# Kernel optimization log

Measured on AMD Instinct MI355X. Metric: run time of the kernel, lower is better.

## Reference

```python
import jax, jax.numpy as jnp
import numpy as np

C = 256; NH = 8; HD = C // NH; NL = 4; NP = 4; DFF = 1024
B = 8; NQ = 900
SHAPES = ((100, 100), (50, 50), (25, 25), (13, 13))
LEN = sum(h * w for h, w in SHAPES)


def setup_inputs() -> dict:
    key = jax.random.key(0)
    ks = jax.random.split(key, 16)
    s = 0.02
    d = {}
    d['tgt'] = jax.random.normal(ks[0], (B, NQ, C), jnp.float32)
    d['query_pos'] = jax.random.normal(ks[1], (B, NQ, C), jnp.float32)
    d['reference_points'] = jax.random.uniform(ks[2], (B, NQ, NL, 2), jnp.float32)
    d['src'] = jax.random.normal(ks[3], (B, LEN, C), jnp.float32)
    d['spatial_shapes'] = np.array(SHAPES, dtype=np.int32)
    # self-attn (nn.MultiheadAttention) params, stored [in,out]
    d['sa_in_w'] = jax.random.normal(ks[4], (C, 3 * C), jnp.float32) * s
    d['sa_in_b'] = jnp.zeros((3 * C,), jnp.float32)
    d['sa_out_w'] = jax.random.normal(ks[5], (C, C), jnp.float32) * s
    d['sa_out_b'] = jnp.zeros((C,), jnp.float32)
    d['ln2_g'] = jnp.ones((C,), jnp.float32); d['ln2_b'] = jnp.zeros((C,), jnp.float32)
    # MSDeformAttn params
    d['off_w'] = jax.random.normal(ks[6], (C, NH * NL * NP * 2), jnp.float32) * s
    d['off_b'] = jax.random.normal(ks[7], (NH * NL * NP * 2,), jnp.float32) * 0.5
    d['attw_w'] = jax.random.normal(ks[8], (C, NH * NL * NP), jnp.float32) * s
    d['attw_b'] = jnp.zeros((NH * NL * NP,), jnp.float32)
    d['val_w'] = jax.random.normal(ks[9], (C, C), jnp.float32) * s
    d['val_b'] = jnp.zeros((C,), jnp.float32)
    d['proj_w'] = jax.random.normal(ks[10], (C, C), jnp.float32) * s
    d['proj_b'] = jnp.zeros((C,), jnp.float32)
    d['ln1_g'] = jnp.ones((C,), jnp.float32); d['ln1_b'] = jnp.zeros((C,), jnp.float32)
    # FFN
    d['lin1_w'] = jax.random.normal(ks[11], (C, DFF), jnp.float32) * s
    d['lin1_b'] = jnp.zeros((DFF,), jnp.float32)
    d['lin2_w'] = jax.random.normal(ks[12], (DFF, C), jnp.float32) * s
    d['lin2_b'] = jnp.zeros((C,), jnp.float32)
    d['ln3_g'] = jnp.ones((C,), jnp.float32); d['ln3_b'] = jnp.zeros((C,), jnp.float32)
    return d


def _ln(x, g, b):
    m = jnp.mean(x, -1, keepdims=True)
    v = jnp.mean((x - m) ** 2, -1, keepdims=True)
    return (x - m) * jax.lax.rsqrt(v + 1e-5) * g + b


def _bilinear(v, loc, H, W):
    # v: [B,NH,H*W,HD]; loc: [B,NQ,NH,NP,2] normalized to [0,1]
    # matches F.grid_sample(align_corners=False, padding_mode='zeros')
    b = v.shape[0]; nq = loc.shape[1]
    x = loc[..., 0] * W - 0.5
    y = loc[..., 1] * H - 0.5
    x0 = jnp.floor(x); y0 = jnp.floor(y)
    dx = x - x0; dy = y - y0
    x0i = x0.astype(jnp.int32); y0i = y0.astype(jnp.int32)

    def gat(ix, iy):
        valid = ((ix >= 0) & (ix < W) & (iy >= 0) & (iy < H)).astype(v.dtype)
        idx = jnp.clip(iy, 0, H - 1) * W + jnp.clip(ix, 0, W - 1)  # [B,NQ,NH,NP]
        idx_t = jnp.transpose(idx, (0, 2, 1, 3)).reshape(b, NH, nq * NP)
        g = jnp.take_along_axis(v, idx_t[..., None], axis=2).reshape(b, NH, nq, NP, HD)
        return g * jnp.transpose(valid, (0, 2, 1, 3))[..., None]

    wt = lambda a: jnp.transpose(a, (0, 2, 1, 3))[..., None]
    return (gat(x0i, y0i) * wt((1 - dx) * (1 - dy))
            + gat(x0i + 1, y0i) * wt(dx * (1 - dy))
            + gat(x0i, y0i + 1) * wt((1 - dx) * dy)
            + gat(x0i + 1, y0i + 1) * wt(dx * dy))


def _msda(q, ref, src, shapes, val_w, val_b, off_w, off_b, attw_w, attw_b, proj_w, proj_b):
    b, nq, _ = q.shape
    value = jnp.transpose((src @ val_w + val_b).reshape(b, -1, NH, HD), (0, 2, 1, 3))  # [B,NH,Len,HD]
    off = (q @ off_w + off_b).reshape(b, nq, NH, NL, NP, 2)
    aw = jax.nn.softmax((q @ attw_w + attw_b).reshape(b, nq, NH, NL * NP), -1)
    aw = aw.reshape(b, nq, NH, NL, NP)
    acc = jnp.zeros((b, NH, nq, HD), q.dtype)
    start = 0
    for l, (H_, W_) in enumerate(shapes):
        norm = jnp.array([W_, H_], q.dtype)
        loc = ref[:, :, None, l, None, :] + off[:, :, :, l] / norm  # [B,NQ,NH,NP,2]
        smp = _bilinear(value[:, :, start:start + H_ * W_], loc, H_, W_)  # [B,NH,NQ,NP,HD]
        acc = acc + jnp.sum(smp * jnp.transpose(aw[:, :, :, l], (0, 2, 1, 3))[..., None], axis=3)
        start += H_ * W_
    out = jnp.transpose(acc, (0, 2, 1, 3)).reshape(b, nq, C)
    return out @ proj_w + proj_b


def _self_attn(x, pos, in_w, in_b, out_w, out_b):
    b, nq, _ = x.shape
    qk = x + pos
    q = (qk @ in_w[:, :C] + in_b[:C]).reshape(b, nq, NH, HD)
    k = (qk @ in_w[:, C:2 * C] + in_b[C:2 * C]).reshape(b, nq, NH, HD)
    v = (x @ in_w[:, 2 * C:] + in_b[2 * C:]).reshape(b, nq, NH, HD)
    att = jax.nn.softmax(jnp.einsum('bqhd,bkhd->bhqk', q, k) * (1.0 / float(np.sqrt(HD))), -1)
    o = jnp.einsum('bhqk,bkhd->bqhd', att, v).reshape(b, nq, C)
    return o @ out_w + out_b


def _forward(tgt, query_pos, reference_points, src, shapes,
             sa_in_w, sa_in_b, sa_out_w, sa_out_b, ln2_g, ln2_b,
             off_w, off_b, attw_w, attw_b, val_w, val_b, proj_w, proj_b, ln1_g, ln1_b,
             lin1_w, lin1_b, lin2_w, lin2_b, ln3_g, ln3_b):
    t2 = _self_attn(tgt, query_pos, sa_in_w, sa_in_b, sa_out_w, sa_out_b)
    t = _ln(tgt + t2, ln2_g, ln2_b)
    t2 = _msda(t + query_pos, reference_points, src, shapes,
               val_w, val_b, off_w, off_b, attw_w, attw_b, proj_w, proj_b)
    t = _ln(t + t2, ln1_g, ln1_b)
    h = jax.nn.relu(t @ lin1_w + lin1_b) @ lin2_w + lin2_b
    return _ln(t + h, ln3_g, ln3_b)


def reference(tgt, query_pos, reference_points, src, spatial_shapes,
              sa_in_w, sa_in_b, sa_out_w, sa_out_b, ln2_g, ln2_b,
              off_w, off_b, attw_w, attw_b, val_w, val_b, proj_w, proj_b, ln1_g, ln1_b,
              lin1_w, lin1_b, lin2_w, lin2_b, ln3_g, ln3_b):
    shapes = [(int(h), int(w)) for h, w in np.asarray(spatial_shapes)]
    return _forward(tgt, query_pos, reference_points, src, shapes,
                    sa_in_w, sa_in_b, sa_out_w, sa_out_b, ln2_g, ln2_b,
                    off_w, off_b, attw_w, attw_b, val_w, val_b, proj_w, proj_b, ln1_g, ln1_b,
                    lin1_w, lin1_b, lin2_w, lin2_b, ln3_g, ln3_b)
```

## Files before the change

### kernel.cpp

```cpp
#include <hip/hip_runtime.h>
#include <hip/hip_bf16.h>
#include <type_traits>

#define C_DIM 256
#define NHEAD 8
#define HDIM 32
#define NLVL 4
#define NPT 4
#define DFF_DIM 1024
#define BB 8
#define NQ_DIM 900
#define LEN_DIM 13294
#define ROWS (BB * NQ_DIM)
#define VROWS (BB * LEN_DIM)
#define VT_LD 928

typedef __attribute__((ext_vector_type(8))) short short8v;
typedef __attribute__((ext_vector_type(8))) unsigned short ushort8v;
typedef __attribute__((ext_vector_type(4))) float float4v;
typedef __attribute__((ext_vector_type(4))) unsigned short ushort4v;

__device__ __forceinline__ float bf2f(unsigned short u) {
  union { unsigned int i; float f; } v; v.i = ((unsigned int)u) << 16; return v.f;
}
__device__ __forceinline__ unsigned short f2bf(float f) {
  __hip_bfloat16 h = __float2bfloat16(f);
  return *reinterpret_cast<unsigned short*>(&h);
}

#define WCONV_BLOCKS 2048
__global__ __launch_bounds__(256) void wprep_kernel(
    const float* __restrict__ w0, const float* __restrict__ w1,
    const float* __restrict__ w2, const float* __restrict__ w3,
    const float* __restrict__ w4, const float* __restrict__ w5,
    const float* __restrict__ w6, const float* __restrict__ w7,
    unsigned short* __restrict__ out,
    const float* __restrict__ tgt, const float* __restrict__ qpos,
    unsigned short* __restrict__ tgtbf, unsigned short* __restrict__ x0bf, int n4) {
  int bid = blockIdx.x;
  if (bid < WCONV_BLOCKS) {
    const int Ks[8] = {256, 256, 256, 256, 256, 256, 256, 1024};
    const int Ns[8] = {768, 256, 256, 128, 256, 256, 1024, 256};
    const int Oo[8] = {0, 196608, 262144, 327680, 360448, 425984, 491520, 753664};
    int w = bid >> 8, bx = bid & 255;
    int K = Ks[w], N = Ns[w];
    int ntx = N >> 5, nty = K >> 5;
    if (bx >= ntx * nty) return;
    int tx = bx % ntx, ty = bx / ntx;
    const float* W = w == 0 ? w0 : w == 1 ? w1 : w == 2 ? w2 : w == 3 ? w3
                   : w == 4 ? w4 : w == 5 ? w5 : w == 6 ? w6 : w7;
    __shared__ float tile[32][33];
    int c = threadIdx.x & 31, rg = threadIdx.x >> 5;
#pragma unroll
    for (int j = 0; j < 4; ++j) {
      int k = ty * 32 + rg * 4 + j;
      tile[rg * 4 + j][c] = W[(size_t)k * N + tx * 32 + c];
    }
    __syncthreads();
    unsigned short* o = out + Oo[w];
#pragma unroll
    for (int j = 0; j < 4; ++j) {
      int n = tx * 32 + rg * 4 + j;
      o[(size_t)n * K + ty * 32 + c] = f2bf(tile[c][rg * 4 + j]);
    }
  } else {
    int i = (bid - WCONV_BLOCKS) * 256 + threadIdx.x;
    if (i < n4) {
      float4 x = reinterpret_cast<const float4*>(tgt)[i];
      float4 y = reinterpret_cast<const float4*>(qpos)[i];
      ushort4v u1, u2;
      u1[0] = f2bf(x.x); u1[1] = f2bf(x.y); u1[2] = f2bf(x.z); u1[3] = f2bf(x.w);
      u2[0] = f2bf(x.x + y.x); u2[1] = f2bf(x.y + y.y);
      u2[2] = f2bf(x.z + y.z); u2[3] = f2bf(x.w + y.w);
      *reinterpret_cast<ushort4v*>(tgtbf + (size_t)i * 4) = u1;
      *reinterpret_cast<ushort4v*>(x0bf + (size_t)i * 4) = u2;
    }
  }
}

template <typename TA, typename TO, int RELU, int VT>
__device__ __forceinline__ void gemm_body(
    unsigned short* smem,
    const TA* __restrict__ A, const TA* __restrict__ A2,
    const unsigned short* __restrict__ Wt,
    const float* __restrict__ bias, const float* __restrict__ bias2,
    TO* __restrict__ Cout, TO* __restrict__ Cout2,
    int M, int N, int K, int lda, int ldc, int ldc2, int colSplit,
    int bx, int by) {
  auto Al = reinterpret_cast<unsigned short(*)[128][40]>(smem);
  auto Wl = reinterpret_cast<unsigned short(*)[128][40]>(smem + 10240);
  const int tid = threadIdx.x;
  const int lane = tid & 63, wid = tid >> 6;
  const int g = lane >> 4, ql = lane & 15;
  const int wr = wid >> 1, wc = wid & 1;
  const int row0 = by * 128, col0 = bx * 128;

  const TA* Ause = (A2 != nullptr && col0 >= colSplit) ? A2 : A;

  float4v acc[4][4];
#pragma unroll
  for (int i = 0; i < 4; ++i)
#pragma unroll
    for (int j = 0; j < 4; ++j) acc[i][j] = (float4v){0.f, 0.f, 0.f, 0.f};

  float4 areg_f[4];
  ushort8v areg_b[2];
  ushort8v wreg[2];

  auto loadA = [&](int k0) {
    if constexpr (std::is_same<TA, float>::value) {
#pragma unroll
      for (int j = 0; j < 4; ++j) {
        int c = tid + 256 * j;
        int row = c >> 3, f4 = c & 7;
        int gr = min(row0 + row, M - 1);
        areg_f[j] = *reinterpret_cast<const float4*>(Ause + (size_t)gr * lda + k0 + f4 * 4);
      }
    } else {
#pragma unroll
      for (int j = 0; j < 2; ++j) {
        int c = tid + 256 * j;
        int row = c >> 2, ch = c & 3;
        int gr = min(row0 + row, M - 1);
        areg_b[j] = *reinterpret_cast<const ushort8v*>(
            reinterpret_cast<const unsigned short*>(Ause) + (size_t)gr * lda + k0 + ch * 8);
      }
    }
  };
  auto loadW = [&](int k0) {
#pragma unroll
    for (int j = 0; j < 2; ++j) {
      int c = tid + 256 * j;
      int row = c >> 2, ch = c & 3;
      wreg[j] = *reinterpret_cast<const ushort8v*>(
          Wt + (size_t)(col0 + row) * K + k0 + ch * 8);
    }
  };
  auto storeA = [&](int buf) {
    if constexpr (std::is_same<TA, float>::value) {
#pragma unroll
      for (int j = 0; j < 4; ++j) {
        int c = tid + 256 * j;
        int row = c >> 3, f4 = c & 7;
        ushort4v u;
        u[0] = f2bf(areg_f[j].x); u[1] = f2bf(areg_f[j].y);
        u[2] = f2bf(areg_f[j].z); u[3] = f2bf(areg_f[j].w);
        *reinterpret_cast<ushort4v*>(&Al[buf][row][f4 * 4]) = u;
      }
    } else {
#pragma unroll
      for (int j = 0; j < 2; ++j) {
        int c = tid + 256 * j;
        int row = c >> 2, ch = c & 3;
        *reinterpret_cast<ushort8v*>(&Al[buf][row][ch * 8]) = areg_b[j];
      }
    }
  };
  auto storeW = [&](int buf) {
#pragma unroll
    for (int j = 0; j < 2; ++j) {
      int c = tid + 256 * j;
      int row = c >> 2, ch = c & 3;
      *reinterpret_cast<ushort8v*>(&Wl[buf][row][ch * 8]) = wreg[j];
    }
  };

  const int nt = K >> 5;
  loadA(0); loadW(0);
  storeA(0); storeW(0);

  for (int t = 0; t < nt; ++t) {
    __syncthreads();
    if (t + 1 < nt) { loadA((t + 1) << 5); loadW((t + 1) << 5); }
    const int cur = t & 1;
    short8v af[4], bfr[4];
#pragma unroll
    for (int mi = 0; mi < 4; ++mi)
      af[mi] = *reinterpret_cast<const short8v*>(&Al[cur][wr * 64 + mi * 16 + ql][8 * g]);
#pragma unroll
    for (int ni = 0; ni < 4; ++ni)
      bfr[ni] = *reinterpret_cast<const short8v*>(&Wl[cur][wc * 64 + ni * 16 + ql][8 * g]);
#pragma unroll
    for (int mi = 0; mi < 4; ++mi)
#pragma unroll
      for (int ni = 0; ni < 4; ++ni)
        acc[mi][ni] = __builtin_amdgcn_mfma_f32_16x16x32_bf16(af[mi], bfr[ni], acc[mi][ni], 0, 0, 0);
    if (t + 1 < nt) { storeA(cur ^ 1); storeW(cur ^ 1); }
  }

  const bool sel2 = (Cout2 != nullptr && col0 >= colSplit);
  const int cbase = sel2 ? (col0 - colSplit) : col0;
  if (VT && sel2) {
    unsigned short* vTp = reinterpret_cast<unsigned short*>(Cout2);
    float bv[4];
#pragma unroll
    for (int ni = 0; ni < 4; ++ni) bv[ni] = bias2[cbase + wc * 64 + ni * 16 + ql];
#pragma unroll
    for (int mi = 0; mi < 4; ++mi) {
#pragma unroll
      for (int r = 0; r < 4; ++r) {
        int row = row0 + wr * 64 + mi * 16 + 4 * g + r;
        if (row >= M) continue;
        int bb = row / 900, rr = row - bb * 900;
#pragma unroll
        for (int ni = 0; ni < 4; ++ni) {
          int c = cbase + wc * 64 + ni * 16 + ql;
          vTp[((size_t)bb * 256 + c) * VT_LD + rr] = f2bf(acc[mi][ni][r] + bv[ni]);
        }
      }
    }
    return;
  }
  const float* bsrc = sel2 ? bias2 : bias;
  TO* outp = sel2 ? Cout2 : Cout;
  const int ldco = sel2 ? ldc2 : ldc;
  float bv[4];
#pragma unroll
  for (int ni = 0; ni < 4; ++ni) bv[ni] = bsrc[cbase + wc * 64 + ni * 16 + ql];
#pragma unroll
  for (int mi = 0; mi < 4; ++mi) {
#pragma unroll
    for (int r = 0; r < 4; ++r) {
      int row = row0 + wr * 64 + mi * 16 + 4 * g + r;
      if (row >= M) continue;
#pragma unroll
      for (int ni = 0; ni < 4; ++ni) {
        int col = cbase + wc * 64 + ni * 16 + ql;
        float v = acc[mi][ni][r] + bv[ni];
        if (RELU) v = fmaxf(v, 0.f);
        if constexpr (std::is_same<TO, float>::value) {
          outp[(size_t)row * ldco + col] = v;
        } else {
          outp[(size_t)row * ldco + col] = __float2bfloat16(v);
        }
      }
    }
  }
}

template <typename TA, typename TO, int RELU>
__global__ __launch_bounds__(256) void mfma_gemm_kernel(
    const TA* __restrict__ A, const TA* __restrict__ A2,
    const unsigned short* __restrict__ Wt,
    const float* __restrict__ bias, const float* __restrict__ bias2,
    TO* __restrict__ Cout, TO* __restrict__ Cout2,
    int M, int N, int K, int lda, int ldc, int ldc2, int colSplit) {
  __shared__ unsigned short smem[20480];
  gemm_body<TA, TO, RELU, 0>(smem, A, A2, Wt, bias, bias2, Cout, Cout2,
                             M, N, K, lda, ldc, ldc2, colSplit,
                             blockIdx.x, blockIdx.y);
}

#define QKV_BLOCKS (6 * 57)
__global__ __launch_bounds__(256) void qkv_value_kernel(
    const unsigned short* __restrict__ x0bf, const unsigned short* __restrict__ tgtbf,
    const unsigned short* __restrict__ sa_inT, const float* __restrict__ sa_in_b,
    __hip_bfloat16* __restrict__ qkbuf, __hip_bfloat16* __restrict__ vT,
    const float* __restrict__ src, const unsigned short* __restrict__ valT,
    const float* __restrict__ val_b, __hip_bfloat16* __restrict__ value) {
  __shared__ unsigned short smem[20480];
  int bid = blockIdx.x;
  if (bid < QKV_BLOCKS) {
    gemm_body<unsigned short, __hip_bfloat16, 0, 1>(
        smem, x0bf, tgtbf, sa_inT, sa_in_b, sa_in_b + 512, qkbuf, vT,
        ROWS, 768, 256, 256, 512, 0, 512, bid % 6, bid / 6);
  } else {
    int t = bid - QKV_BLOCKS;
    gemm_body<float, __hip_bfloat16, 0, 0>(
        smem, src, nullptr, valT, val_b, nullptr, value, nullptr,
        VROWS, 256, 256, 256, 256, 0, 1 << 30, t & 1, t >> 1);
  }
}

__global__ __launch_bounds__(256) void ln_fused_kernel(const float* __restrict__ x,
                                                       const float* __restrict__ y,
                                                       const float* __restrict__ gg,
                                                       const float* __restrict__ bb,
                                                       float* __restrict__ out,
                                                       unsigned short* __restrict__ out2,
                                                       const float* __restrict__ qadd) {
  int row = blockIdx.x, t = threadIdx.x;
  size_t base = (size_t)row * C_DIM + t;
  float v = x[base] + y[base];
  float s = v, s2 = v * v;
#pragma unroll
  for (int o = 32; o > 0; o >>= 1) {
    s += __shfl_xor(s, o);
    s2 += __shfl_xor(s2, o);
  }
  __shared__ float w1[4], w2[4];
  int wid = t >> 6, lane = t & 63;
  if (lane == 0) { w1[wid] = s; w2[wid] = s2; }
  __syncthreads();
  float S = w1[0] + w1[1] + w1[2] + w1[3];
  float S2 = w2[0] + w2[1] + w2[2] + w2[3];
  float mean = S * (1.f / 256.f);
  float var = S2 * (1.f / 256.f) - mean * mean;
  float rstd = rsqrtf(var + 1e-5f);
  float r = (v - mean) * rstd * gg[t] + bb[t];
  out[base] = r;
  if (out2) {
    float r2 = qadd ? (r + qadd[base]) : r;
    out2[base] = f2bf(r2);
  }
}

__global__ __launch_bounds__(256) void self_attn_mfma_kernel(
    const unsigned short* __restrict__ qk, const unsigned short* __restrict__ vT,
    unsigned short* __restrict__ out) {
  __shared__ unsigned short P_lds[4][16][32];
  const int tid = threadIdx.x;
  const int lane = tid & 63, wid = tid >> 6;
  const int g = lane >> 4, ql = lane & 15;
  const int bh = blockIdx.y;
  const int b = bh >> 3, h = bh & 7;
  const int q0 = blockIdx.x * 64 + wid * 16;
  const float scale = 0.17677669529663687f;

  const unsigned short* qk_b = qk + (size_t)b * NQ_DIM * 512;
  const int qrow = min(q0 + ql, NQ_DIM - 1);
  short8v qf = *reinterpret_cast<const short8v*>(
      qk_b + (size_t)qrow * 512 + h * HDIM + 8 * g);
  const unsigned short* kb = qk_b + 256 + h * HDIM + 8 * g;
  const unsigned short* vtb0 = vT + ((size_t)b * 256 + h * HDIM + ql) * VT_LD;
  const unsigned short* vtb1 = vtb0 + 16 * VT_LD;

  float4v o0 = {0.f, 0.f, 0.f, 0.f}, o1 = {0.f, 0.f, 0.f, 0.f};
  float m = -1e30f, lsum = 0.f;

  const int NT = 29;
  for (int kt = 0; kt < NT; ++kt) {
    const int k_base = kt * 32;
    int kr0 = min(k_base + ql, NQ_DIM - 1);
    int kr1 = min(k_base + 16 + ql, NQ_DIM - 1);
    short8v kf0 = *reinterpret_cast<const short8v*>(kb + (size_t)kr0 * 512);
    short8v kf1 = *reinterpret_cast<const short8v*>(kb + (size_t)kr1 * 512);
    float4v z = {0.f, 0.f, 0.f, 0.f};
    float4v s0 = __builtin_amdgcn_mfma_f32_16x16x32_bf16(kf0, qf, z, 0, 0, 0);
    float4v s1 = __builtin_amdgcn_mfma_f32_16x16x32_bf16(kf1, qf, z, 0, 0, 0);

    float s[8];
#pragma unroll
    for (int r = 0; r < 4; ++r) { s[r] = s0[r] * scale; s[4 + r] = s1[r] * scale; }
    if (kt == NT - 1) {
#pragma unroll
      for (int i = 0; i < 8; ++i) {
        int kk = k_base + 16 * (i >> 2) + 4 * g + (i & 3);
        if (kk >= NQ_DIM) s[i] = -1e30f;
      }
    }
    float tm = s[0];
#pragma unroll
    for (int i = 1; i < 8; ++i) tm = fmaxf(tm, s[i]);
    tm = fmaxf(tm, __shfl_xor(tm, 16));
    tm = fmaxf(tm, __shfl_xor(tm, 32));
    float mnew = fmaxf(m, tm);
    float alpha = __expf(m - mnew);
    float p[8];
    float ts = 0.f;
#pragma unroll
    for (int i = 0; i < 8; ++i) { p[i] = __expf(s[i] - mnew); ts += p[i]; }
    ts += __shfl_xor(ts, 16);
    ts += __shfl_xor(ts, 32);
    lsum = lsum * alpha + ts;
    m = mnew;

    ushort4v pp0, pp1;
#pragma unroll
    for (int r = 0; r < 4; ++r) { pp0[r] = f2bf(p[r]); pp1[r] = f2bf(p[4 + r]); }
    *reinterpret_cast<ushort4v*>(&P_lds[wid][ql][4 * g]) = pp0;
    *reinterpret_cast<ushort4v*>(&P_lds[wid][ql][16 + 4 * g]) = pp1;
    asm volatile("s_waitcnt lgkmcnt(0)" ::: "memory");
    __builtin_amdgcn_sched_barrier(0);

    o0 *= alpha;
    o1 *= alpha;

    short8v pf = *reinterpret_cast<const short8v*>(&P_lds[wid][ql][8 * g]);
    short8v vf0 = *reinterpret_cast<const short8v*>(vtb0 + k_base + 8 * g);
    short8v vf1 = *reinterpret_cast<const short8v*>(vtb1 + k_base + 8 * g);
    o0 = __builtin_amdgcn_mfma_f32_16x16x32_bf16(vf0, pf, o0, 0, 0, 0);
    o1 = __builtin_amdgcn_mfma_f32_16x16x32_bf16(vf1, pf, o1, 0, 0, 0);
  }

  float inv = 1.f / lsum;
  if (q0 + ql < NQ_DIM) {
    unsigned short* op = out + ((size_t)(b * NQ_DIM) + q0 + ql) * C_DIM + h * HDIM;
    ushort4v u0, u1;
#pragma unroll
    for (int r = 0; r < 4; ++r) { u0[r] = f2bf(o0[r] * inv); u1[r] = f2bf(o1[r] * inv); }
    *reinterpret_cast<ushort4v*>(op + 4 * g) = u0;
    *reinterpret_cast<ushort4v*>(op + 16 + 4 * g) = u1;
  }
}

__global__ __launch_bounds__(256) void softmax16_kernel(float* __restrict__ aw, int total) {
  int t = blockIdx.x * 256 + threadIdx.x;
  if (t >= total) return;
  float* p = aw + (size_t)t * 16;
  float vals[16];
  float m = -1e30f;
#pragma unroll
  for (int i = 0; i < 16; ++i) { vals[i] = p[i]; m = fmaxf(m, vals[i]); }
  float s = 0.f;
#pragma unroll
  for (int i = 0; i < 16; ++i) { vals[i] = __expf(vals[i] - m); s += vals[i]; }
  float inv = 1.f / s;
#pragma unroll
  for (int i = 0; i < 16; ++i) p[i] = vals[i] * inv;
}

__global__ __launch_bounds__(256) void msda_sample_kernel(
    const unsigned short* __restrict__ value,
    const float* __restrict__ off,
    const float* __restrict__ aw,
    const float* __restrict__ refp,
    const int* __restrict__ shapes,
    unsigned short* __restrict__ out) {
  int g = blockIdx.x * 32 + (threadIdx.x >> 3);
  int d4 = threadIdx.x & 7;
  int h = g & 7;
  int row = g >> 3;
  int b = row / NQ_DIM;
  float acc0 = 0.f, acc1 = 0.f, acc2 = 0.f, acc3 = 0.f;
  int start = 0;
  const float* offr = off + (size_t)row * 256 + h * 32;
  const float* awr  = aw + (size_t)row * 128 + h * 16;
  const float* rpr  = refp + (size_t)row * NLVL * 2;
#pragma unroll
  for (int l = 0; l < NLVL; ++l) {
    int Hl = shapes[2 * l], Wl = shapes[2 * l + 1];
    float fx = rpr[2 * l + 0] * (float)Wl - 0.5f;
    float fy = rpr[2 * l + 1] * (float)Hl - 0.5f;
    const unsigned short* vbase =
        value + ((size_t)(b * LEN_DIM + start)) * C_DIM + h * HDIM + d4 * 4;
#pragma unroll
    for (int p = 0; p < NPT; ++p) {
      float x = fx + offr[l * 8 + p * 2];
      float y = fy + offr[l * 8 + p * 2 + 1];
      float a = awr[l * 4 + p];
      float x0f = floorf(x), y0f = floorf(y);
      float dx = x - x0f, dy = y - y0f;
      int x0 = (int)x0f, y0 = (int)y0f;
      int x1 = x0 + 1, y1 = y0 + 1;
      float wx1 = dx, wx0 = 1.f - dx;
      float wy1 = dy * a, wy0 = (1.f - dy) * a;
      bool vx0 = ((unsigned)x0 < (unsigned)Wl);
      bool vx1 = ((unsigned)x1 < (unsigned)Wl);
      bool vy0 = ((unsigned)y0 < (unsigned)Hl);
      bool vy1 = ((unsigned)y1 < (unsigned)Hl);
      float w00 = (vx0 && vy0) ? wx0 * wy0 : 0.f;
      float w10 = (vx1 && vy0) ? wx1 * wy0 : 0.f;
      float w01 = (vx0 && vy1) ? wx0 * wy1 : 0.f;
      float w11 = (vx1 && vy1) ? wx1 * wy1 : 0.f;
      int x0c = min(max(x0, 0), Wl - 1), x1c = min(max(x1, 0), Wl - 1);
      int y0c = min(max(y0, 0), Hl - 1), y1c = min(max(y1, 0), Hl - 1);
      int r0 = y0c * Wl, r1 = y1c * Wl;
      ushort4v g00 = *reinterpret_cast<const ushort4v*>(vbase + ((r0 + x0c) << 8));
      ushort4v g10 = *reinterpret_cast<const ushort4v*>(vbase + ((r0 + x1c) << 8));
      ushort4v g01 = *reinterpret_cast<const ushort4v*>(vbase + ((r1 + x0c) << 8));
      ushort4v g11 = *reinterpret_cast<const ushort4v*>(vbase + ((r1 + x1c) << 8));
      acc0 += w00 * bf2f(g00[0]) + w10 * bf2f(g10[0]) + w01 * bf2f(g01[0]) + w11 * bf2f(g11[0]);
      acc1 += w00 * bf2f(g00[1]) + w10 * bf2f(g10[1]) + w01 * bf2f(g01[1]) + w11 * bf2f(g11[1]);
      acc2 += w00 * bf2f(g00[2]) + w10 * bf2f(g10[2]) + w01 * bf2f(g01[2]) + w11 * bf2f(g11[2]);
      acc3 += w00 * bf2f(g00[3]) + w10 * bf2f(g10[3]) + w01 * bf2f(g01[3]) + w11 * bf2f(g11[3]);
    }
    start += Hl * Wl;
  }
  ushort4v o;
  o[0] = f2bf(acc0); o[1] = f2bf(acc1); o[2] = f2bf(acc2); o[3] = f2bf(acc3);
  *reinterpret_cast<ushort4v*>(out + (size_t)row * C_DIM + h * HDIM + d4 * 4) = o;
}

extern "C" void kernel_launch(void* const* d_in, const int* in_sizes, int n_in,
                              void* d_out, int out_size, void* d_ws, size_t ws_size,
                              hipStream_t stream) {
  const float* tgt      = (const float*)d_in[0];
  const float* qpos     = (const float*)d_in[1];
  const float* refp     = (const float*)d_in[2];
  const float* src      = (const float*)d_in[3];
  const int*   shapes   = (const int*)d_in[4];
  const float* sa_in_w  = (const float*)d_in[5];
  const float* sa_in_b  = (const float*)d_in[6];
  const float* sa_out_w = (const float*)d_in[7];
  const float* sa_out_b = (const float*)d_in[8];
  const float* ln2_g    = (const float*)d_in[9];
  const float* ln2_b    = (const float*)d_in[10];
  const float* off_w    = (const float*)d_in[11];
  const float* off_b    = (const float*)d_in[12];
  const float* attw_w   = (const float*)d_in[13];
  const float* attw_b   = (const float*)d_in[14];
  const float* val_w    = (const float*)d_in[15];
  const float* val_b    = (const float*)d_in[16];
  const float* proj_w   = (const float*)d_in[17];
  const float* proj_b   = (const float*)d_in[18];
  const float* ln1_g    = (const float*)d_in[19];
  const float* ln1_b    = (const float*)d_in[20];
  const float* lin1_w   = (const float*)d_in[21];
  const float* lin1_b   = (const float*)d_in[22];
  const float* lin2_w   = (const float*)d_in[23];
  const float* lin2_b   = (const float*)d_in[24];
  const float* ln3_g    = (const float*)d_in[25];
  const float* ln3_b    = (const float*)d_in[26];

  char* ws = (char*)d_ws;
  size_t off_b_ws = 0;
  auto alloc = [&](size_t bytes) {
    char* p = ws + off_b_ws;
    off_b_ws += (bytes + 255) & ~(size_t)255;
    return p;
  };
  unsigned short* wT     = (unsigned short*)alloc((size_t)1015808 * 2);
  unsigned short* value  = (unsigned short*)alloc((size_t)VROWS * C_DIM * 2);
  unsigned short* qkbuf  = (unsigned short*)alloc((size_t)ROWS * 512 * 2);
  unsigned short* vTbuf  = (unsigned short*)alloc((size_t)BB * 256 * VT_LD * 2);
  unsigned short* tgtbf  = (unsigned short*)alloc((size_t)ROWS * C_DIM * 2);
  unsigned short* X0bf   = (unsigned short*)alloc((size_t)ROWS * C_DIM * 2);
  unsigned short* attnbf = (unsigned short*)alloc((size_t)ROWS * C_DIM * 2);
  unsigned short* X3bf   = (unsigned short*)alloc((size_t)ROWS * C_DIM * 2);
  unsigned short* sampbf = (unsigned short*)alloc((size_t)ROWS * C_DIM * 2);
  unsigned short* X6bf   = (unsigned short*)alloc((size_t)ROWS * C_DIM * 2);
  unsigned short* hidbf  = (unsigned short*)alloc((size_t)ROWS * DFF_DIM * 2);
  float* X1 = (float*)alloc((size_t)ROWS * C_DIM * 4);
  float* X2 = (float*)alloc((size_t)ROWS * C_DIM * 4);
  float* X4 = (float*)alloc((size_t)ROWS * C_DIM * 4);
  float* X5 = (float*)alloc((size_t)ROWS * 128 * 4);
  float* X6 = (float*)alloc((size_t)ROWS * C_DIM * 4);
  if (off_b_ws > ws_size) return;

  unsigned short* sa_inT = wT + 0;
  unsigned short* sa_outT = wT + 196608;
  unsigned short* offT   = wT + 262144;
  unsigned short* valT   = wT + 360448;
  unsigned short* projT  = wT + 425984;
  unsigned short* lin1T  = wT + 491520;
  unsigned short* lin2T  = wT + 753664;

  dim3 blk(256);
  const int MB7200 = (ROWS + 127) / 128;
  const int MBV = (VROWS + 127) / 128;
  int n4 = ROWS * C_DIM / 4;
  int prepBlocks = (n4 + 255) / 256;

  wprep_kernel<<<WCONV_BLOCKS + prepBlocks, blk, 0, stream>>>(
      sa_in_w, sa_out_w, off_w, attw_w, val_w, proj_w, lin1_w, lin2_w, wT,
      tgt, qpos, tgtbf, X0bf, n4);

  qkv_value_kernel<<<QKV_BLOCKS + 2 * MBV, blk, 0, stream>>>(
      X0bf, tgtbf, sa_inT, sa_in_b, (__hip_bfloat16*)qkbuf, (__hip_bfloat16*)vTbuf,
      src, valT, val_b, (__hip_bfloat16*)value);

  self_attn_mfma_kernel<<<dim3(15, 64), blk, 0, stream>>>(qkbuf, vTbuf, attnbf);
  mfma_gemm_kernel<unsigned short, float, 0><<<dim3(2, MB7200), blk, 0, stream>>>(
      attnbf, nullptr, sa_outT, sa_out_b, nullptr,
      X1, nullptr, ROWS, 256, 256, 256, 256, 0, 1 << 30);
  ln_fused_kernel<<<ROWS, blk, 0, stream>>>(tgt, X1, ln2_g, ln2_b, X2, X3bf, qpos);

  mfma_gemm_kernel<unsigned short, float, 0><<<dim3(3, MB7200), blk, 0, stream>>>(
      X3bf, nullptr, offT, off_b, attw_b,
      X4, X5, ROWS, 384, 256, 256, 256, 128, 256);
  softmax16_kernel<<<(ROWS * NHEAD + 255) / 256, blk, 0, stream>>>(X5, ROWS * NHEAD);
  msda_sample_kernel<<<ROWS * NHEAD / 32, blk, 0, stream>>>(
      value, X4, X5, refp, shapes, sampbf);
  mfma_gemm_kernel<unsigned short, float, 0><<<dim3(2, MB7200), blk, 0, stream>>>(
      sampbf, nullptr, projT, proj_b, nullptr,
      X1, nullptr, ROWS, 256, 256, 256, 256, 0, 1 << 30);
  ln_fused_kernel<<<ROWS, blk, 0, stream>>>(X2, X1, ln1_g, ln1_b, X6, X6bf, nullptr);

  mfma_gemm_kernel<unsigned short, __hip_bfloat16, 1><<<dim3(8, MB7200), blk, 0, stream>>>(
      X6bf, nullptr, lin1T, lin1_b, nullptr,
      (__hip_bfloat16*)hidbf, nullptr, ROWS, 1024, 256, 256, 1024, 0, 1 << 30);
  mfma_gemm_kernel<unsigned short, float, 0><<<dim3(2, MB7200), blk, 0, stream>>>(
      hidbf, nullptr, lin2T, lin2_b, nullptr,
      X1, nullptr, ROWS, 256, 1024, 1024, 256, 0, 1 << 30);
  ln_fused_kernel<<<ROWS, blk, 0, stream>>>(X6, X1, ln3_g, ln3_b, (float*)d_out, nullptr, nullptr);
}
```

Baseline: 231.9 us.

## Split V transpose into tiled kernel and widen MSDA gathers to 8 channels

The QKV GEMM epilogue used to scatter V straight into a transposed layout with strided 2-byte stores. It now writes V row-major and a separate LDS-tiled transpose kernel builds vT with coalesced accesses. Separately, the deformable-attention sampler now has each thread gather 8 bf16 channels per corner instead of 4, which halves the thread count and launches half as many blocks. The costs are an extra kernel launch, an extra buffer round trip for V, and more registers per sampling thread.

Result: faster. 225.6 us (-2.7%).

```diff
diff --git a/kernel.cpp b/kernel.cpp
--- a/kernel.cpp
+++ b/kernel.cpp
@@ -78,7 +78,7 @@
   }
 }
 
-template <typename TA, typename TO, int RELU, int VT>
+template <typename TA, typename TO, int RELU>
 __device__ __forceinline__ void gemm_body(
     unsigned short* smem,
     const TA* __restrict__ A, const TA* __restrict__ A2,
@@ -189,31 +189,10 @@
   }
 
   const bool sel2 = (Cout2 != nullptr && col0 >= colSplit);
-  const int cbase = sel2 ? (col0 - colSplit) : col0;
-  if (VT && sel2) {
-    unsigned short* vTp = reinterpret_cast<unsigned short*>(Cout2);
-    float bv[4];
-#pragma unroll
-    for (int ni = 0; ni < 4; ++ni) bv[ni] = bias2[cbase + wc * 64 + ni * 16 + ql];
-#pragma unroll
-    for (int mi = 0; mi < 4; ++mi) {
-#pragma unroll
-      for (int r = 0; r < 4; ++r) {
-        int row = row0 + wr * 64 + mi * 16 + 4 * g + r;
-        if (row >= M) continue;
-        int bb = row / 900, rr = row - bb * 900;
-#pragma unroll
-        for (int ni = 0; ni < 4; ++ni) {
-          int c = cbase + wc * 64 + ni * 16 + ql;
-          vTp[((size_t)bb * 256 + c) * VT_LD + rr] = f2bf(acc[mi][ni][r] + bv[ni]);
-        }
-      }
-    }
-    return;
-  }
   const float* bsrc = sel2 ? bias2 : bias;
   TO* outp = sel2 ? Cout2 : Cout;
   const int ldco = sel2 ? ldc2 : ldc;
+  const int cbase = sel2 ? (col0 - colSplit) : col0;
   float bv[4];
 #pragma unroll
   for (int ni = 0; ni < 4; ++ni) bv[ni] = bsrc[cbase + wc * 64 + ni * 16 + ql];
@@ -246,30 +225,51 @@
     TO* __restrict__ Cout, TO* __restrict__ Cout2,
     int M, int N, int K, int lda, int ldc, int ldc2, int colSplit) {
   __shared__ unsigned short smem[20480];
-  gemm_body<TA, TO, RELU, 0>(smem, A, A2, Wt, bias, bias2, Cout, Cout2,
-                             M, N, K, lda, ldc, ldc2, colSplit,
-                             blockIdx.x, blockIdx.y);
+  gemm_body<TA, TO, RELU>(smem, A, A2, Wt, bias, bias2, Cout, Cout2,
+                          M, N, K, lda, ldc, ldc2, colSplit,
+                          blockIdx.x, blockIdx.y);
 }
 
 #define QKV_BLOCKS (6 * 57)
 __global__ __launch_bounds__(256) void qkv_value_kernel(
     const unsigned short* __restrict__ x0bf, const unsigned short* __restrict__ tgtbf,
     const unsigned short* __restrict__ sa_inT, const float* __restrict__ sa_in_b,
-    __hip_bfloat16* __restrict__ qkbuf, __hip_bfloat16* __restrict__ vT,
+    __hip_bfloat16* __restrict__ qkbuf, __hip_bfloat16* __restrict__ vbuf,
     const float* __restrict__ src, const unsigned short* __restrict__ valT,
     const float* __restrict__ val_b, __hip_bfloat16* __restrict__ value) {
   __shared__ unsigned short smem[20480];
   int bid = blockIdx.x;
   if (bid < QKV_BLOCKS) {
-    gemm_body<unsigned short, __hip_bfloat16, 0, 1>(
-        smem, x0bf, tgtbf, sa_inT, sa_in_b, sa_in_b + 512, qkbuf, vT,
-        ROWS, 768, 256, 256, 512, 0, 512, bid % 6, bid / 6);
+    gemm_body<unsigned short, __hip_bfloat16, 0>(
+        smem, x0bf, tgtbf, sa_inT, sa_in_b, sa_in_b + 512, qkbuf, vbuf,
+        ROWS, 768, 256, 256, 512, 256, 512, bid % 6, bid / 6);
   } else {
     int t = bid - QKV_BLOCKS;
-    gemm_body<float, __hip_bfloat16, 0, 0>(
+    gemm_body<float, __hip_bfloat16, 0>(
         smem, src, nullptr, valT, val_b, nullptr, value, nullptr,
         VROWS, 256, 256, 256, 256, 0, 1 << 30, t & 1, t >> 1);
   }
+}
+
+__global__ __launch_bounds__(256) void vtrans_kernel(
+    const unsigned short* __restrict__ vbuf, unsigned short* __restrict__ vT) {
+  __shared__ unsigned short tile[32][34];
+  int b = blockIdx.y;
+  int ct = blockIdx.x & 7;
+  int rt = blockIdx.x >> 3;
+  int rl = threadIdx.x >> 3, c4 = (threadIdx.x & 7) * 4;
+  int gr = min(rt * 32 + rl, NQ_DIM - 1);
+  ushort4v v = *reinterpret_cast<const ushort4v*>(
+      vbuf + ((size_t)(b * NQ_DIM + gr)) * 256 + ct * 32 + c4);
+  tile[rl][c4] = v[0]; tile[rl][c4 + 1] = v[1];
+  tile[rl][c4 + 2] = v[2]; tile[rl][c4 + 3] = v[3];
+  __syncthreads();
+  int cl = threadIdx.x >> 3, r4 = (threadIdx.x & 7) * 4;
+  ushort4v o;
+  o[0] = tile[r4][cl]; o[1] = tile[r4 + 1][cl];
+  o[2] = tile[r4 + 2][cl]; o[3] = tile[r4 + 3][cl];
+  *reinterpret_cast<ushort4v*>(
+      vT + ((size_t)b * 256 + ct * 32 + cl) * VT_LD + rt * 32 + r4) = o;
 }
 
 __global__ __launch_bounds__(256) void ln_fused_kernel(const float* __restrict__ x,
@@ -417,12 +417,12 @@
     const float* __restrict__ refp,
     const int* __restrict__ shapes,
     unsigned short* __restrict__ out) {
-  int g = blockIdx.x * 32 + (threadIdx.x >> 3);
-  int d4 = threadIdx.x & 7;
+  int g = blockIdx.x * 64 + (threadIdx.x >> 2);
+  int d8 = threadIdx.x & 3;
   int h = g & 7;
   int row = g >> 3;
   int b = row / NQ_DIM;
-  float acc0 = 0.f, acc1 = 0.f, acc2 = 0.f, acc3 = 0.f;
+  float acc[8] = {};
   int start = 0;
   const float* offr = off + (size_t)row * 256 + h * 32;
   const float* awr  = aw + (size_t)row * 128 + h * 16;
@@ -433,7 +433,7 @@
     float fx = rpr[2 * l + 0] * (float)Wl - 0.5f;
     float fy = rpr[2 * l + 1] * (float)Hl - 0.5f;
     const unsigned short* vbase =
-        value + ((size_t)(b * LEN_DIM + start)) * C_DIM + h * HDIM + d4 * 4;
+        value + ((size_t)(b * LEN_DIM + start)) * C_DIM + h * HDIM + d8 * 8;
 #pragma unroll
     for (int p = 0; p < NPT; ++p) {
       float x = fx + offr[l * 8 + p * 2];
@@ -456,20 +456,21 @@
       int x0c = min(max(x0, 0), Wl - 1), x1c = min(max(x1, 0), Wl - 1);
       int y0c = min(max(y0, 0), Hl - 1), y1c = min(max(y1, 0), Hl - 1);
       int r0 = y0c * Wl, r1 = y1c * Wl;
-      ushort4v g00 = *reinterpret_cast<const ushort4v*>(vbase + ((r0 + x0c) << 8));
-      ushort4v g10 = *reinterpret_cast<const ushort4v*>(vbase + ((r0 + x1c) << 8));
-      ushort4v g01 = *reinterpret_cast<const ushort4v*>(vbase + ((r1 + x0c) << 8));
-      ushort4v g11 = *reinterpret_cast<const ushort4v*>(vbase + ((r1 + x1c) << 8));
-      acc0 += w00 * bf2f(g00[0]) + w10 * bf2f(g10[0]) + w01 * bf2f(g01[0]) + w11 * bf2f(g11[0]);
-      acc1 += w00 * bf2f(g00[1]) + w10 * bf2f(g10[1]) + w01 * bf2f(g01[1]) + w11 * bf2f(g11[1]);
-      acc2 += w00 * bf2f(g00[2]) + w10 * bf2f(g10[2]) + w01 * bf2f(g01[2]) + w11 * bf2f(g11[2]);
-      acc3 += w00 * bf2f(g00[3]) + w10 * bf2f(g10[3]) + w01 * bf2f(g01[3]) + w11 * bf2f(g11[3]);
+      ushort8v g00 = *reinterpret_cast<const ushort8v*>(vbase + ((r0 + x0c) << 8));
+      ushort8v g10 = *reinterpret_cast<const ushort8v*>(vbase + ((r0 + x1c) << 8));
+      ushort8v g01 = *reinterpret_cast<const ushort8v*>(vbase + ((r1 + x0c) << 8));
+      ushort8v g11 = *reinterpret_cast<const ushort8v*>(vbase + ((r1 + x1c) << 8));
+#pragma unroll
+      for (int j = 0; j < 8; ++j)
+        acc[j] += w00 * bf2f(g00[j]) + w10 * bf2f(g10[j]) +
+                  w01 * bf2f(g01[j]) + w11 * bf2f(g11[j]);
     }
     start += Hl * Wl;
   }
-  ushort4v o;
-  o[0] = f2bf(acc0); o[1] = f2bf(acc1); o[2] = f2bf(acc2); o[3] = f2bf(acc3);
-  *reinterpret_cast<ushort4v*>(out + (size_t)row * C_DIM + h * HDIM + d4 * 4) = o;
+  ushort8v o;
+#pragma unroll
+  for (int j = 0; j < 8; ++j) o[j] = f2bf(acc[j]);
+  *reinterpret_cast<ushort8v*>(out + (size_t)row * C_DIM + h * HDIM + d8 * 8) = o;
 }
 
 extern "C" void kernel_launch(void* const* d_in, const int* in_sizes, int n_in,
@@ -513,6 +514,7 @@
   unsigned short* wT     = (unsigned short*)alloc((size_t)1015808 * 2);
   unsigned short* value  = (unsigned short*)alloc((size_t)VROWS * C_DIM * 2);
   unsigned short* qkbuf  = (unsigned short*)alloc((size_t)ROWS * 512 * 2);
+  unsigned short* vbuf   = (unsigned short*)alloc((size_t)ROWS * 256 * 2);
   unsigned short* vTbuf  = (unsigned short*)alloc((size_t)BB * 256 * VT_LD * 2);
   unsigned short* tgtbf  = (unsigned short*)alloc((size_t)ROWS * C_DIM * 2);
   unsigned short* X0bf   = (unsigned short*)alloc((size_t)ROWS * C_DIM * 2);
@@ -547,8 +549,10 @@
       tgt, qpos, tgtbf, X0bf, n4);
 
   qkv_value_kernel<<<QKV_BLOCKS + 2 * MBV, blk, 0, stream>>>(
-      X0bf, tgtbf, sa_inT, sa_in_b, (__hip_bfloat16*)qkbuf, (__hip_bfloat16*)vTbuf,
+      X0bf, tgtbf, sa_inT, sa_in_b, (__hip_bfloat16*)qkbuf, (__hip_bfloat16*)vbuf,
       src, valT, val_b, (__hip_bfloat16*)value);
+
+  vtrans_kernel<<<dim3(8 * 29, BB), blk, 0, stream>>>(vbuf, vTbuf);
 
   self_attn_mfma_kernel<<<dim3(15, 64), blk, 0, stream>>>(qkbuf, vTbuf, attnbf);
   mfma_gemm_kernel<unsigned short, float, 0><<<dim3(2, MB7200), blk, 0, stream>>>(
@@ -560,7 +564,7 @@
       X3bf, nullptr, offT, off_b, attw_b,
       X4, X5, ROWS, 384, 256, 256, 256, 128, 256);
   softmax16_kernel<<<(ROWS * NHEAD + 255) / 256, blk, 0, stream>>>(X5, ROWS * NHEAD);
-  msda_sample_kernel<<<ROWS * NHEAD / 32, blk, 0, stream>>>(
+  msda_sample_kernel<<<ROWS * NHEAD / 64, blk, 0, stream>>>(
       value, X4, X5, refp, shapes, sampbf);
   mfma_gemm_kernel<unsigned short, float, 0><<<dim3(2, MB7200), blk, 0, stream>>>(
       sampbf, nullptr, projT, proj_b, nullptr,
```
